# Optimization experiments

Measured on AMD Instinct MI355X. Metric: run time of the kernel, lower is better.

Reference implementation:

```python
import jax, jax.numpy as jnp
import numpy as np

EPS = 1e-5
STRIDE = 4
NSAMPLE = 8


def _fps(p, m):
    # furthest point sampling on one cloud p:[n,3] -> int32 indices [m]
    d0 = jnp.sum((p - p[0]) ** 2, axis=-1)
    def step(dist, _):
        nxt = jnp.argmax(dist).astype(jnp.int32)
        d = jnp.sum((p - p[nxt]) ** 2, axis=-1)
        return jnp.minimum(dist, d), nxt
    _, idxs = jax.lax.scan(step, d0, None, length=m - 1)
    return jnp.concatenate([jnp.zeros((1,), jnp.int32), idxs])


def _bn(x, gamma, beta):
    # inference-mode BatchNorm1d with running_mean=0, running_var=1
    return gamma * x / jnp.sqrt(1.0 + EPS) + beta


def _transition_down(p, x, W, gamma, beta):
    # p:[B,n,3], x:[B,n,C]  (stride>1 path of TransitionDown)
    B, n, _ = p.shape
    m = n // STRIDE
    pc = jax.lax.stop_gradient(p)
    idx = jax.vmap(_fps, in_axes=(0, None))(pc, m)              # [B,m]
    n_p = jnp.take_along_axis(p, idx[:, :, None], axis=1)       # [B,m,3]
    npc = jax.lax.stop_gradient(n_p)
    # squared distances sampled->all points, [B,m,n] (no [B,m,n,3] temp)
    d2 = (jnp.sum(npc ** 2, -1)[:, :, None]
          + jnp.sum(pc ** 2, -1)[:, None, :]
          - 2.0 * jnp.einsum('bmd,bnd->bmn', npc, pc))
    _, knn = jax.lax.top_k(-d2, NSAMPLE)                        # [B,m,k]
    gp = jax.vmap(lambda pb, kb: pb[kb])(p, knn)                # [B,m,k,3]
    gx = jax.vmap(lambda xb, kb: xb[kb])(x, knn)                # [B,m,k,C]
    rel = gp - n_p[:, :, None, :]                               # use_xyz=True
    feat = jnp.concatenate([rel, gx], axis=-1)                  # [B,m,k,3+C]
    y = jax.nn.relu(_bn(feat @ W, gamma, beta))
    return n_p, jnp.max(y, axis=2)                              # MaxPool1d(k)


def setup_inputs():
    key = jax.random.key(0)
    ks = jax.random.split(key, 16)
    B, n = 8, 8192
    N = B * n
    inp = {
        'p0': jax.random.normal(ks[0], (N, 3), jnp.float32),
        'x0': jax.random.normal(ks[1], (N, 3), jnp.float32),
        'o0': (jnp.arange(1, B + 1) * n).astype(jnp.int32),
    }
    dims_in = [6, 3 + 32, 3 + 64, 3 + 128, 3 + 256]
    dims_out = [32, 64, 128, 256, 512]
    for i in range(5):
        s = 1.0 / np.sqrt(dims_in[i])
        inp[f'W{i+1}'] = jax.random.uniform(ks[2 + i], (dims_in[i], dims_out[i]), jnp.float32, -s, s)
        inp[f'g{i+1}'] = jnp.ones((dims_out[i],), jnp.float32)
        inp[f'b{i+1}'] = jnp.zeros((dims_out[i],), jnp.float32)
    s1 = 1.0 / np.sqrt(512.0)
    inp['Wc1'] = jax.random.uniform(ks[8], (512, 256), jnp.float32, -s1, s1)
    inp['bc1'] = jax.random.uniform(ks[9], (256,), jnp.float32, -s1, s1)
    inp['gcls'] = jnp.ones((256,), jnp.float32)
    inp['bcls'] = jnp.zeros((256,), jnp.float32)
    s2 = 1.0 / np.sqrt(256.0)
    inp['Wc2'] = jax.random.uniform(ks[10], (256, 40), jnp.float32, -s2, s2)
    inp['bc2'] = jax.random.uniform(ks[11], (40,), jnp.float32, -s2, s2)
    return inp


def reference(p0, x0, o0, W1, g1, b1, W2, g2, b2, W3, g3, b3, W4, g4, b4,
              W5, g5, b5, Wc1, bc1, gcls, bcls, Wc2, bc2):
    B = o0.shape[0]
    n = p0.shape[0] // B  # equal-size segments
    p = p0.reshape(B, n, 3)
    x = jnp.concatenate([p0, x0], axis=1).reshape(B, n, 6)  # c=6: cat(xyz, feat)
    # enc1: stride 1 -> relu(bn(linear(x)))
    x = jax.nn.relu(_bn(x @ W1, g1, b1))
    # enc2..enc5: FPS + KNN group + linear/bn/relu + maxpool over neighbors
    p, x = _transition_down(p, x, W2, g2, b2)
    p, x = _transition_down(p, x, W3, g3, b3)
    p, x = _transition_down(p, x, W4, g4, b4)
    p, x = _transition_down(p, x, W5, g5, b5)
    # offset-based segment mean pooling (equal segments -> mean over axis 1)
    pooled = jnp.mean(x, axis=1)                               # [B,512]
    h = jax.nn.relu(_bn(pooled @ Wc1 + bc1, gcls, bcls))       # dropout eval=id
    return h @ Wc2 + bc2                                       # [B,40]
```

## Files before the change

### kernel.cpp

```cpp
#include <hip/hip_runtime.h>
#include <float.h>

#define BNI 0.9999950000374997f

__device__ __forceinline__ float sq3(float x, float y, float z) {
  return __fadd_rn(__fadd_rn(__fmul_rn(x, x), __fmul_rn(y, y)), __fmul_rn(z, z));
}

__device__ __forceinline__ int key_idx(double k) {
  return ~__double2loint(k);
}

template <int CTRL>
__device__ __forceinline__ double dpp_max(double k) {
  union { double d; int i[2]; } u, r;
  u.d = k;
  r.i[0] = __builtin_amdgcn_mov_dpp(u.i[0], CTRL, 0xF, 0xF, true);
  r.i[1] = __builtin_amdgcn_mov_dpp(u.i[1], CTRL, 0xF, 0xF, true);
  return fmax(k, r.d);
}
__device__ __forceinline__ double swz16_max(double k) {
  union { double d; int i[2]; } u, r;
  u.d = k;
  r.i[0] = __builtin_amdgcn_ds_swizzle(u.i[0], 0x401F);
  r.i[1] = __builtin_amdgcn_ds_swizzle(u.i[1], 0x401F);
  return fmax(k, r.d);
}
__device__ __forceinline__ double bperm32_max(double k, int lane) {
  union { double d; int i[2]; } u, r;
  u.d = k;
  int addr = ((lane ^ 32) << 2);
  r.i[0] = __builtin_amdgcn_ds_bpermute(addr, u.i[0]);
  r.i[1] = __builtin_amdgcn_ds_bpermute(addr, u.i[1]);
  return fmax(k, r.d);
}
__device__ __forceinline__ double wave_max_key(double k, int lane) {
  k = dpp_max<0xB1>(k);
  k = dpp_max<0x4E>(k);
  k = dpp_max<0x141>(k);
  k = dpp_max<0x140>(k);
  k = swz16_max(k);
  k = bperm32_max(k, lane);
  return k;
}

__global__ void k_prep(const float* __restrict__ p, float4* __restrict__ P4, int N) {
  int i = blockIdx.x * blockDim.x + threadIdx.x;
  if (i < N) {
    float x = p[3 * i], y = p[3 * i + 1], z = p[3 * i + 2];
    P4[i] = make_float4(x, y, z, sq3(x, y, z));
  }
}

__global__ __launch_bounds__(256) void k_enc1(
    const float* __restrict__ p0, const float* __restrict__ x0,
    const float* __restrict__ W, const float* __restrict__ g, const float* __restrict__ bt,
    float* __restrict__ X, int N) {
  int t = blockIdx.x * 256 + threadIdx.x;
  int pt = t >> 5, c = t & 31;
  if (pt >= N) return;
  float i0 = p0[pt * 3], i1 = p0[pt * 3 + 1], i2 = p0[pt * 3 + 2];
  float i3 = x0[pt * 3], i4 = x0[pt * 3 + 1], i5 = x0[pt * 3 + 2];
  float a = i0 * W[c] + i1 * W[32 + c] + i2 * W[64 + c] +
            i3 * W[96 + c] + i4 * W[128 + c] + i5 * W[160 + c];
  a = a * (g[c] * BNI) + bt[c];
  X[(size_t)pt * 32 + c] = fmaxf(a, 0.f);
}

__device__ __forceinline__ unsigned mpart3(unsigned x) {
  return (x & 1u) | ((x & 2u) << 2) | ((x & 4u) << 4);
}
__device__ __forceinline__ int cell_id(float4 v, const float* __restrict__ bb) {
  int cx = min(max((int)((v.x - bb[0]) * bb[3]), 0), 7);
  int cy = min(max((int)((v.y - bb[1]) * bb[4]), 0), 7);
  int cz = min(max((int)((v.z - bb[2]) * bb[5]), 0), 7);
  return (int)((mpart3(cx) << 2) | (mpart3(cy) << 1) | mpart3(cz));
}

__global__ __launch_bounds__(256) void k_bbox(const float4* __restrict__ P, int n,
                                              float* __restrict__ bb) {
  __shared__ float sm[6][4];
  int b = blockIdx.x, tid = threadIdx.x, lane = tid & 63, wid = tid >> 6;
  const float4* Pb = P + (size_t)b * n;
  float lx = FLT_MAX, hx = -FLT_MAX, ly = FLT_MAX, hy = -FLT_MAX, lz = FLT_MAX, hz = -FLT_MAX;
  for (int i = tid; i < n; i += 256) {
    float4 v = Pb[i];
    lx = fminf(lx, v.x); hx = fmaxf(hx, v.x);
    ly = fminf(ly, v.y); hy = fmaxf(hy, v.y);
    lz = fminf(lz, v.z); hz = fmaxf(hz, v.z);
  }
#pragma unroll
  for (int off = 1; off < 64; off <<= 1) {
    lx = fminf(lx, __shfl_xor(lx, off)); hx = fmaxf(hx, __shfl_xor(hx, off));
    ly = fminf(ly, __shfl_xor(ly, off)); hy = fmaxf(hy, __shfl_xor(hy, off));
    lz = fminf(lz, __shfl_xor(lz, off)); hz = fmaxf(hz, __shfl_xor(hz, off));
  }
  if (lane == 0) {
    sm[0][wid] = lx; sm[1][wid] = hx; sm[2][wid] = ly;
    sm[3][wid] = hy; sm[4][wid] = lz; sm[5][wid] = hz;
  }
  __syncthreads();
  if (tid == 0) {
    float LX = fminf(fminf(sm[0][0], sm[0][1]), fminf(sm[0][2], sm[0][3]));
    float HX = fmaxf(fmaxf(sm[1][0], sm[1][1]), fmaxf(sm[1][2], sm[1][3]));
    float LY = fminf(fminf(sm[2][0], sm[2][1]), fminf(sm[2][2], sm[2][3]));
    float HY = fmaxf(fmaxf(sm[3][0], sm[3][1]), fmaxf(sm[3][2], sm[3][3]));
    float LZ = fminf(fminf(sm[4][0], sm[4][1]), fminf(sm[4][2], sm[4][3]));
    float HZ = fmaxf(fmaxf(sm[5][0], sm[5][1]), fmaxf(sm[5][2], sm[5][3]));
    float ex = HX - LX, ey = HY - LY, ez = HZ - LZ;
    float* o = bb + b * 8;
    o[0] = LX; o[1] = LY; o[2] = LZ;
    o[3] = ex > 0.f ? 8.f / ex : 0.f;
    o[4] = ey > 0.f ? 8.f / ey : 0.f;
    o[5] = ez > 0.f ? 8.f / ez : 0.f;
  }
}

__global__ void k_hist(const float4* __restrict__ P, const float* __restrict__ bb,
                       int* __restrict__ hist, int n, int total) {
  int i = blockIdx.x * blockDim.x + threadIdx.x;
  if (i >= total) return;
  int b = i / n;
  int cid = cell_id(P[i], bb + b * 8);
  atomicAdd(&hist[b * 512 + cid], 1);
}

__global__ __launch_bounds__(512) void k_scan(const int* __restrict__ hist,
                                              int* __restrict__ cursor) {
  __shared__ int s[512];
  int b = blockIdx.x, t = threadIdx.x;
  int h = hist[b * 512 + t];
  s[t] = h;
  __syncthreads();
  for (int d = 1; d < 512; d <<= 1) {
    int v = (t >= d) ? s[t - d] : 0;
    __syncthreads();
    s[t] += v;
    __syncthreads();
  }
  cursor[b * 512 + t] = s[t] - h;
}

__global__ void k_scatter(const float4* __restrict__ P, const float* __restrict__ bb,
                          int* __restrict__ cursor, float4* __restrict__ Psort,
                          int n, int total) {
  int i = blockIdx.x * blockDim.x + threadIdx.x;
  if (i >= total) return;
  int b = i / n, il = i - b * n;
  float4 v = P[i];
  int cid = cell_id(v, bb + b * 8);
  int pos = atomicAdd(&cursor[b * 512 + cid], 1);
  Psort[(size_t)b * n + pos] = make_float4(v.x, v.y, v.z, __int_as_float(il));
}

template <int PT, int NW>
__global__ __launch_bounds__(64 * NW) void k_fps(
    const float4* __restrict__ Psort, const float4* __restrict__ Porig,
    int n, int m, int* __restrict__ out_idx) {
  __shared__ double keys[2][NW];
  const int b = blockIdx.x;
  const int tid = threadIdx.x;
  const int lane = tid & 63, wid = tid >> 6;
  const float4* PS = Psort + (size_t)b * n;
  const float4* PO = Porig + (size_t)b * n;

  float px[PT], py[PT], pz[PT], dist[PT];
  int ni[PT];
  const int base = wid * (64 * PT);
#pragma unroll
  for (int k = 0; k < PT; ++k) {
    float4 v = PS[base + k * 64 + lane];
    px[k] = v.x; py[k] = v.y; pz[k] = v.z;
    ni[k] = ~__float_as_int(v.w);
  }
  float lx = px[0], hx = px[0], ly = py[0], hy = py[0], lz = pz[0], hz = pz[0];
#pragma unroll
  for (int k = 1; k < PT; ++k) {
    lx = fminf(lx, px[k]); hx = fmaxf(hx, px[k]);
    ly = fminf(ly, py[k]); hy = fmaxf(hy, py[k]);
    lz = fminf(lz, pz[k]); hz = fmaxf(hz, pz[k]);
  }
#pragma unroll
  for (int off = 1; off < 64; off <<= 1) {
    lx = fminf(lx, __shfl_xor(lx, off)); hx = fmaxf(hx, __shfl_xor(hx, off));
    ly = fminf(ly, __shfl_xor(ly, off)); hy = fmaxf(hy, __shfl_xor(hy, off));
    lz = fminf(lz, __shfl_xor(lz, off)); hz = fmaxf(hz, __shfl_xor(hz, off));
  }
  if (tid == 0) out_idx[(size_t)b * m] = 0;

  float4 q = PO[0];
  double lk = -1.0;
#pragma unroll
  for (int k = 0; k < PT; ++k) {
    float dx = __fsub_rn(px[k], q.x), dy = __fsub_rn(py[k], q.y), dz = __fsub_rn(pz[k], q.z);
    float d = sq3(dx, dy, dz);
    dist[k] = d;
    lk = fmax(lk, __hiloint2double(__float_as_int(d), ni[k]));
  }
  double wkey = wave_max_key(lk, lane);

  for (int t = 1; t < m; ++t) {
    int buf = t & 1;
    if (lane == 0) keys[buf][wid] = wkey;
    __syncthreads();
    double kb = keys[buf][lane & (NW - 1)];
    if (NW >= 2)  kb = dpp_max<0xB1>(kb);
    if (NW >= 4)  kb = dpp_max<0x4E>(kb);
    if (NW >= 8)  kb = dpp_max<0x141>(kb);
    if (NW >= 16) kb = dpp_max<0x140>(kb);
    int wi = key_idx(kb);
    if (tid == 0) out_idx[(size_t)b * m + t] = wi;
    if (t + 1 >= m) break;
    float4 qq = PO[wi];
    float tx = fmaxf(fmaxf(__fsub_rn(lx, qq.x), __fsub_rn(qq.x, hx)), 0.f);
    float ty = fmaxf(fmaxf(__fsub_rn(ly, qq.y), __fsub_rn(qq.y, hy)), 0.f);
    float tz = fmaxf(fmaxf(__fsub_rn(lz, qq.z), __fsub_rn(qq.z, hz)), 0.f);
    float lb = sq3(tx, ty, tz);
    float wv = __uint_as_float((unsigned)__double2hiint(wkey));
    if (lb < wv) {
      double lk2 = -1.0;
#pragma unroll
      for (int k = 0; k < PT; ++k) {
        float dx = __fsub_rn(px[k], qq.x), dy = __fsub_rn(py[k], qq.y), dz = __fsub_rn(pz[k], qq.z);
        float d = sq3(dx, dy, dz);
        float nd = fminf(dist[k], d);
        dist[k] = nd;
        lk2 = fmax(lk2, __hiloint2double(__float_as_int(nd), ni[k]));
      }
      wkey = wave_max_key(lk2, lane);
    }
  }
}

__global__ void k_gather(const float4* __restrict__ Pin, const int* __restrict__ idx,
                         float4* __restrict__ Pout, int n, int m, int total) {
  int t = blockIdx.x * blockDim.x + threadIdx.x;
  if (t >= total) return;
  int b = t / m;
  Pout[t] = Pin[(size_t)b * n + idx[t]];
}

__global__ __launch_bounds__(256) void k_knn(
    const float4* __restrict__ Pq, const float4* __restrict__ Pc,
    int n, int m, int* __restrict__ knn) {
  int gw = (blockIdx.x * 256 + threadIdx.x) >> 6;
  int lane = threadIdx.x & 63;
  int b = gw / m;
  float4 q = Pq[gw];
  const float4* C = Pc + (size_t)b * n;
  float ad[8];
  int ai[8];
#pragma unroll
  for (int s = 0; s < 8; ++s) { ad[s] = FLT_MAX; ai[s] = 0x7fffffff; }
  for (int j = lane; j < n; j += 64) {
    float4 c = C[j];
    float dot = __fadd_rn(__fadd_rn(__fmul_rn(q.x, c.x), __fmul_rn(q.y, c.y)), __fmul_rn(q.z, c.z));
    float d2 = __fsub_rn(__fadd_rn(q.w, c.w), __fmul_rn(2.f, dot));
    if (d2 < ad[7] || (d2 == ad[7] && j < ai[7])) {
      float cd = d2; int ci = j;
#pragma unroll
      for (int s = 0; s < 8; ++s) {
        bool sw = (cd < ad[s]) || (cd == ad[s] && ci < ai[s]);
        float td = ad[s]; int ti = ai[s];
        ad[s] = sw ? cd : td; ai[s] = sw ? ci : ti;
        cd = sw ? td : cd;  ci = sw ? ti : ci;
      }
    }
  }
  int pos = 0;
  int* kout = knn + (size_t)gw * 8;
#pragma unroll
  for (int r = 0; r < 8; ++r) {
    float hv = FLT_MAX; int hi = 0x7fffffff;
#pragma unroll
    for (int s = 7; s >= 0; --s)
      if (pos == s) { hv = ad[s]; hi = ai[s]; }
    float v = hv; int ix = hi;
#pragma unroll
    for (int off = 1; off < 64; off <<= 1) {
      float ov = __shfl_xor(v, off);
      int oi = __shfl_xor(ix, off);
      if (ov < v || (ov == v && oi < ix)) { v = ov; ix = oi; }
    }
    if (hv == v && hi == ix) pos++;
    if (lane == 0) kout[r] = ix;
  }
}

template <int CINF, int COUT>
__global__ __launch_bounds__(COUT) void k_feat(
    const float4* __restrict__ Pq, const float4* __restrict__ Pc,
    const float* __restrict__ Xin, const int* __restrict__ knn,
    const float* __restrict__ W, const float* __restrict__ g, const float* __restrict__ bt,
    float* __restrict__ Xout, int n, int m) {
  constexpr int F = 3 + CINF;
  __shared__ float sf[8][F];
  int bi = blockIdx.x;
  int b = bi / m;
  int tid = threadIdx.x;
  float4 q = Pq[bi];
  const int* kn = knn + (size_t)bi * 8;
  if (tid < 8) {
    int nb = kn[tid];
    float4 c = Pc[(size_t)b * n + nb];
    sf[tid][0] = c.x - q.x;
    sf[tid][1] = c.y - q.y;
    sf[tid][2] = c.z - q.z;
  }
  for (int e = tid; e < 8 * CINF; e += COUT) {
    int k = e / CINF, j = e - k * CINF;
    int nb = kn[k];
    sf[k][3 + j] = Xin[((size_t)b * n + nb) * CINF + j];
  }
  __syncthreads();
  int c = tid;
  float acc[8] = {0.f, 0.f, 0.f, 0.f, 0.f, 0.f, 0.f, 0.f};
  for (int j = 0; j < F; ++j) {
    float w = W[(size_t)j * COUT + c];
#pragma unroll
    for (int k = 0; k < 8; ++k) acc[k] = fmaf(sf[k][j], w, acc[k]);
  }
  float sc = g[c] * BNI, bb = bt[c];
  float mx = 0.f;
#pragma unroll
  for (int k = 0; k < 8; ++k) mx = fmaxf(mx, fmaf(acc[k], sc, bb));
  Xout[(size_t)bi * COUT + c] = mx;
}

__global__ __launch_bounds__(512) void k_head(
    const float* __restrict__ X5, const float* __restrict__ Wc1, const float* __restrict__ bc1,
    const float* __restrict__ gc, const float* __restrict__ bcl,
    const float* __restrict__ Wc2, const float* __restrict__ bc2,
    float* __restrict__ out, int m5) {
  __shared__ float sp[512];
  __shared__ float sh[256];
  int b = blockIdx.x, tid = threadIdx.x;
  float s = 0.f;
  for (int i = 0; i < m5; ++i) s += X5[((size_t)b * m5 + i) * 512 + tid];
  sp[tid] = s * (1.0f / m5);
  __syncthreads();
  if (tid < 256) {
    float a = bc1[tid];
    for (int j = 0; j < 512; ++j) a = fmaf(sp[j], Wc1[j * 256 + tid], a);
    a = a * (gc[tid] * BNI) + bcl[tid];
    sh[tid] = fmaxf(a, 0.f);
  }
  __syncthreads();
  if (tid < 40) {
    float a = bc2[tid];
    for (int j = 0; j < 256; ++j) a = fmaf(sh[j], Wc2[j * 40 + tid], a);
    out[b * 40 + tid] = a;
  }
}

extern "C" void kernel_launch(void* const* d_in, const int* in_sizes, int n_in,
                              void* d_out, int out_size, void* d_ws, size_t ws_size,
                              hipStream_t stream) {
  const float* p0 = (const float*)d_in[0];
  const float* x0 = (const float*)d_in[1];
  const int B = in_sizes[2];
  const int N = in_sizes[0] / 3;
  const int n = N / B;
  const float* W1 = (const float*)d_in[3];
  const float* g1 = (const float*)d_in[4];
  const float* b1 = (const float*)d_in[5];
  const float* W2 = (const float*)d_in[6];
  const float* g2 = (const float*)d_in[7];
  const float* b2 = (const float*)d_in[8];
  const float* W3 = (const float*)d_in[9];
  const float* g3 = (const float*)d_in[10];
  const float* b3 = (const float*)d_in[11];
  const float* W4 = (const float*)d_in[12];
  const float* g4 = (const float*)d_in[13];
  const float* b4 = (const float*)d_in[14];
  const float* W5 = (const float*)d_in[15];
  const float* g5 = (const float*)d_in[16];
  const float* b5 = (const float*)d_in[17];
  const float* Wc1 = (const float*)d_in[18];
  const float* bc1 = (const float*)d_in[19];
  const float* gcls = (const float*)d_in[20];
  const float* bcls = (const float*)d_in[21];
  const float* Wc2 = (const float*)d_in[22];
  const float* bc2 = (const float*)d_in[23];
  float* out = (float*)d_out;

  const int m2 = n / 4, m3 = m2 / 4, m4 = m3 / 4, m5 = m4 / 4;

  char* ws = (char*)d_ws;
  size_t off = 0;
  auto alloc = [&](size_t bytes) -> void* {
    void* p = ws + off;
    off += (bytes + 255) & ~(size_t)255;
    return p;
  };
  float4* P2 = (float4*)alloc((size_t)N * 16);
  float* X1 = (float*)alloc((size_t)N * 32 * 4);
  float4* P3 = (float4*)alloc((size_t)B * m2 * 16);
  float4* P4s = (float4*)alloc((size_t)B * m3 * 16);
  float4* P5 = (float4*)alloc((size_t)B * m4 * 16);
  float4* P6 = (float4*)alloc((size_t)B * m5 * 16);
  int* fpsI = (int*)alloc((size_t)B * m2 * 4);
  int* knnI = (int*)alloc((size_t)B * m2 * 8 * 4);
  float* X2 = (float*)alloc((size_t)B * m2 * 64 * 4);
  float* X3 = (float*)alloc((size_t)B * m3 * 128 * 4);
  float* X4 = (float*)alloc((size_t)B * m4 * 256 * 4);
  float* X5 = (float*)alloc((size_t)B * m5 * 512 * 4);
  float4* Psort = (float4*)alloc((size_t)N * 16);
  float* bbox = (float*)alloc((size_t)B * 8 * 4);
  int* hist = (int*)alloc((size_t)B * 512 * 4);
  int* cursor = (int*)alloc((size_t)B * 512 * 4);

  auto sort_stage = [&](const float4* P, int ns) {
    int total = B * ns;
    hipMemsetAsync(hist, 0, (size_t)B * 512 * 4, stream);
    k_bbox<<<B, 256, 0, stream>>>(P, ns, bbox);
    k_hist<<<(total + 255) / 256, 256, 0, stream>>>(P, bbox, hist, ns, total);
    k_scan<<<B, 512, 0, stream>>>(hist, cursor);
    k_scatter<<<(total + 255) / 256, 256, 0, stream>>>(P, bbox, cursor, Psort, ns, total);
  };

  k_prep<<<(N + 255) / 256, 256, 0, stream>>>(p0, P2, N);
  k_enc1<<<(N * 32 + 255) / 256, 256, 0, stream>>>(p0, x0, W1, g1, b1, X1, N);

  sort_stage(P2, n);
  k_fps<8, 16><<<B, 1024, 0, stream>>>(Psort, P2, n, m2, fpsI);
  k_gather<<<(B * m2 + 255) / 256, 256, 0, stream>>>(P2, fpsI, P3, n, m2, B * m2);
  k_knn<<<(B * m2) / 4, 256, 0, stream>>>(P3, P2, n, m2, knnI);
  k_feat<32, 64><<<B * m2, 64, 0, stream>>>(P3, P2, X1, knnI, W2, g2, b2, X2, n, m2);

  sort_stage(P3, m2);
  k_fps<4, 8><<<B, 512, 0, stream>>>(Psort, P3, m2, m3, fpsI);
  k_gather<<<(B * m3 + 255) / 256, 256, 0, stream>>>(P3, fpsI, P4s, m2, m3, B * m3);
  k_knn<<<(B * m3) / 4, 256, 0, stream>>>(P4s, P3, m2, m3, knnI);
  k_feat<64, 128><<<B * m3, 128, 0, stream>>>(P4s, P3, X2, knnI, W3, g3, b3, X3, m2, m3);

  sort_stage(P4s, m3);
  k_fps<2, 4><<<B, 256, 0, stream>>>(Psort, P4s, m3, m4, fpsI);
  k_gather<<<(B * m4 + 255) / 256, 256, 0, stream>>>(P4s, fpsI, P5, m3, m4, B * m4);
  k_knn<<<(B * m4) / 4, 256, 0, stream>>>(P5, P4s, m3, m4, knnI);
  k_feat<128, 256><<<B * m4, 256, 0, stream>>>(P5, P4s, X3, knnI, W4, g4, b4, X4, m3, m4);

  sort_stage(P5, m4);
  k_fps<1, 2><<<B, 128, 0, stream>>>(Psort, P5, m4, m5, fpsI);
  k_gather<<<(B * m5 + 255) / 256, 256, 0, stream>>>(P5, fpsI, P6, m4, m5, B * m5);
  k_knn<<<(B * m5) / 4, 256, 0, stream>>>(P6, P5, m4, m5, knnI);
  k_feat<256, 512><<<B * m5, 512, 0, stream>>>(P6, P5, X4, knnI, W5, g5, b5, X5, m4, m5);

  k_head<<<B, 512, 0, stream>>>(X5, Wc1, bc1, gcls, bcls, Wc2, bc2, out, m5);
}
```

Baseline: 2.621 ms.

## Carry winner coordinates through LDS in FPS and use permlane swaps

The FPS loop now tracks each lane's argmax coordinates and broadcasts the wave winner's xyz into shared memory with its key. This removes the dependent global load of the selected point (PO[wi]) from the serial critical path of every iteration. The cross-row wave reduction uses permlane16/32 swap instructions in place of ds_swizzle and ds_bpermute, and the selected indices are buffered in LDS and written out once at the end. The cost is extra registers and selects in the inner loop, plus a fixed 2048-entry sidx array, which assumes m <= 2048.

```diff
diff --git a/kernel.cpp b/kernel.cpp
--- a/kernel.cpp
+++ b/kernel.cpp
@@ -3,13 +3,12 @@
 
 #define BNI 0.9999950000374997f
 
+typedef unsigned int v2u __attribute__((ext_vector_type(2)));
+
 __device__ __forceinline__ float sq3(float x, float y, float z) {
   return __fadd_rn(__fadd_rn(__fmul_rn(x, x), __fmul_rn(y, y)), __fmul_rn(z, z));
 }
 
-__device__ __forceinline__ int key_idx(double k) {
-  return ~__double2loint(k);
-}
 
 template <int CTRL>
 __device__ __forceinline__ double dpp_max(double k) {
@@ -19,28 +18,29 @@
   r.i[1] = __builtin_amdgcn_mov_dpp(u.i[1], CTRL, 0xF, 0xF, true);
   return fmax(k, r.d);
 }
-__device__ __forceinline__ double swz16_max(double k) {
-  union { double d; int i[2]; } u, r;
-  u.d = k;
-  r.i[0] = __builtin_amdgcn_ds_swizzle(u.i[0], 0x401F);
-  r.i[1] = __builtin_amdgcn_ds_swizzle(u.i[1], 0x401F);
-  return fmax(k, r.d);
-}
-__device__ __forceinline__ double bperm32_max(double k, int lane) {
-  union { double d; int i[2]; } u, r;
-  u.d = k;
-  int addr = ((lane ^ 32) << 2);
-  r.i[0] = __builtin_amdgcn_ds_bpermute(addr, u.i[0]);
-  r.i[1] = __builtin_amdgcn_ds_bpermute(addr, u.i[1]);
-  return fmax(k, r.d);
-}
-__device__ __forceinline__ double wave_max_key(double k, int lane) {
+__device__ __forceinline__ double pl16_kmax(double k) {
+  union { double d; unsigned i[2]; } u; u.d = k;
+  v2u a0 = __builtin_amdgcn_permlane16_swap(u.i[0], u.i[0], false, false);
+  v2u a1 = __builtin_amdgcn_permlane16_swap(u.i[1], u.i[1], false, false);
+  k = fmax(k, __hiloint2double((int)a1[0], (int)a0[0]));
+  k = fmax(k, __hiloint2double((int)a1[1], (int)a0[1]));
+  return k;
+}
+__device__ __forceinline__ double pl32_kmax(double k) {
+  union { double d; unsigned i[2]; } u; u.d = k;
+  v2u a0 = __builtin_amdgcn_permlane32_swap(u.i[0], u.i[0], false, false);
+  v2u a1 = __builtin_amdgcn_permlane32_swap(u.i[1], u.i[1], false, false);
+  k = fmax(k, __hiloint2double((int)a1[0], (int)a0[0]));
+  k = fmax(k, __hiloint2double((int)a1[1], (int)a0[1]));
+  return k;
+}
+__device__ __forceinline__ double wave_kmax(double k) {
   k = dpp_max<0xB1>(k);
   k = dpp_max<0x4E>(k);
   k = dpp_max<0x141>(k);
   k = dpp_max<0x140>(k);
-  k = swz16_max(k);
-  k = bperm32_max(k, lane);
+  k = pl16_kmax(k);
+  k = pl32_kmax(k);
   return k;
 }
 
@@ -157,7 +157,9 @@
 __global__ __launch_bounds__(64 * NW) void k_fps(
     const float4* __restrict__ Psort, const float4* __restrict__ Porig,
     int n, int m, int* __restrict__ out_idx) {
-  __shared__ double keys[2][NW];
+  __shared__ double skey[2][NW];
+  __shared__ float4 scrd[2][NW];
+  __shared__ int sidx[2048];
   const int b = blockIdx.x;
   const int tid = threadIdx.x;
   const int lane = tid & 63, wid = tid >> 6;
@@ -186,50 +188,80 @@
     ly = fminf(ly, __shfl_xor(ly, off)); hy = fmaxf(hy, __shfl_xor(hy, off));
     lz = fminf(lz, __shfl_xor(lz, off)); hz = fmaxf(hz, __shfl_xor(hz, off));
   }
-  if (tid == 0) out_idx[(size_t)b * m] = 0;
-
-  float4 q = PO[0];
+  if (tid == 0) sidx[0] = 0;
+
+  float4 q0 = PO[0];
   double lk = -1.0;
+  float cbx = 0.f, cby = 0.f, cbz = 0.f;
 #pragma unroll
   for (int k = 0; k < PT; ++k) {
-    float dx = __fsub_rn(px[k], q.x), dy = __fsub_rn(py[k], q.y), dz = __fsub_rn(pz[k], q.z);
+    float dx = __fsub_rn(px[k], q0.x), dy = __fsub_rn(py[k], q0.y), dz = __fsub_rn(pz[k], q0.z);
     float d = sq3(dx, dy, dz);
     dist[k] = d;
-    lk = fmax(lk, __hiloint2double(__float_as_int(d), ni[k]));
-  }
-  double wkey = wave_max_key(lk, lane);
+    double cand = __hiloint2double(__float_as_int(d), ni[k]);
+    if (cand > lk) { lk = cand; cbx = px[k]; cby = py[k]; cbz = pz[k]; }
+  }
+  double wk = wave_kmax(lk);
+  {
+    unsigned long long mkm = __ballot(__double_as_longlong(lk) == __double_as_longlong(wk));
+    int wl = (int)__ffsll((long long)mkm) - 1;
+    cbx = __int_as_float(__builtin_amdgcn_readlane(__float_as_int(cbx), wl));
+    cby = __int_as_float(__builtin_amdgcn_readlane(__float_as_int(cby), wl));
+    cbz = __int_as_float(__builtin_amdgcn_readlane(__float_as_int(cbz), wl));
+  }
+  if (lane == 0) {
+    skey[1][wid] = wk;
+    scrd[1][wid] = make_float4(cbx, cby, cbz, 0.f);
+  }
 
   for (int t = 1; t < m; ++t) {
     int buf = t & 1;
-    if (lane == 0) keys[buf][wid] = wkey;
     __syncthreads();
-    double kb = keys[buf][lane & (NW - 1)];
-    if (NW >= 2)  kb = dpp_max<0xB1>(kb);
-    if (NW >= 4)  kb = dpp_max<0x4E>(kb);
-    if (NW >= 8)  kb = dpp_max<0x141>(kb);
-    if (NW >= 16) kb = dpp_max<0x140>(kb);
-    int wi = key_idx(kb);
-    if (tid == 0) out_idx[(size_t)b * m + t] = wi;
+    int rs = lane & (NW - 1);
+    double mine = skey[buf][rs];
+    double ck = mine;
+    if (NW >= 2)  ck = dpp_max<0xB1>(ck);
+    if (NW >= 4)  ck = dpp_max<0x4E>(ck);
+    if (NW >= 8)  ck = dpp_max<0x141>(ck);
+    if (NW >= 16) ck = dpp_max<0x140>(ck);
+    if (tid == 0) sidx[t] = ~__double2loint(ck);
     if (t + 1 >= m) break;
-    float4 qq = PO[wi];
-    float tx = fmaxf(fmaxf(__fsub_rn(lx, qq.x), __fsub_rn(qq.x, hx)), 0.f);
-    float ty = fmaxf(fmaxf(__fsub_rn(ly, qq.y), __fsub_rn(qq.y, hy)), 0.f);
-    float tz = fmaxf(fmaxf(__fsub_rn(lz, qq.z), __fsub_rn(qq.z, hz)), 0.f);
+    unsigned long long wm = __ballot(__double_as_longlong(mine) == __double_as_longlong(ck));
+    int w = (int)__ffsll((long long)wm) - 1;
+    float4 qc = scrd[buf][w];
+    float tx = fmaxf(fmaxf(__fsub_rn(lx, qc.x), __fsub_rn(qc.x, hx)), 0.f);
+    float ty = fmaxf(fmaxf(__fsub_rn(ly, qc.y), __fsub_rn(qc.y, hy)), 0.f);
+    float tz = fmaxf(fmaxf(__fsub_rn(lz, qc.z), __fsub_rn(qc.z, hz)), 0.f);
     float lb = sq3(tx, ty, tz);
-    float wv = __uint_as_float((unsigned)__double2hiint(wkey));
+    float wv = __uint_as_float((unsigned)__double2hiint(wk));
     if (lb < wv) {
       double lk2 = -1.0;
+      float nbx = 0.f, nby = 0.f, nbz = 0.f;
 #pragma unroll
       for (int k = 0; k < PT; ++k) {
-        float dx = __fsub_rn(px[k], qq.x), dy = __fsub_rn(py[k], qq.y), dz = __fsub_rn(pz[k], qq.z);
+        float dx = __fsub_rn(px[k], qc.x), dy = __fsub_rn(py[k], qc.y), dz = __fsub_rn(pz[k], qc.z);
         float d = sq3(dx, dy, dz);
         float nd = fminf(dist[k], d);
         dist[k] = nd;
-        lk2 = fmax(lk2, __hiloint2double(__float_as_int(nd), ni[k]));
+        double cand = __hiloint2double(__float_as_int(nd), ni[k]);
+        if (cand > lk2) { lk2 = cand; nbx = px[k]; nby = py[k]; nbz = pz[k]; }
       }
-      wkey = wave_max_key(lk2, lane);
+      wk = wave_kmax(lk2);
+      unsigned long long mkm = __ballot(__double_as_longlong(lk2) == __double_as_longlong(wk));
+      int wl = (int)__ffsll((long long)mkm) - 1;
+      cbx = __int_as_float(__builtin_amdgcn_readlane(__float_as_int(nbx), wl));
+      cby = __int_as_float(__builtin_amdgcn_readlane(__float_as_int(nby), wl));
+      cbz = __int_as_float(__builtin_amdgcn_readlane(__float_as_int(nbz), wl));
     }
-  }
+    int nbuf = buf ^ 1;
+    if (lane == 0) {
+      skey[nbuf][wid] = wk;
+      scrd[nbuf][wid] = make_float4(cbx, cby, cbz, 0.f);
+    }
+  }
+  __syncthreads();
+  for (int i = tid; i < m; i += 64 * NW)
+    out_idx[(size_t)b * m + i] = sidx[i];
 }
 
 __global__ void k_gather(const float4* __restrict__ Pin, const int* __restrict__ idx,
```

New measurement: 3.016 ms. 1.15x slower.

## Co-schedule FPS with independent KNN/feature work in fused combo kernels

Applied to the files above, without the earlier changes.

Each stage's FPS kernel uses only B blocks and is serial, so the device sits mostly idle while it runs. Independent work (enc1, previous stage's KNN and feature MLP) is folded into the same launch as extra blocks so it runs concurrently with FPS. Feature kernels now also handle multiple queries per block to raise block size. The cost is extra shared memory and register pressure in the fused kernels, which could lower FPS occupancy or let the other blocks compete with FPS for the device.

```diff
diff --git a/kernel.cpp b/kernel.cpp
--- a/kernel.cpp
+++ b/kernel.cpp
@@ -7,9 +7,7 @@
   return __fadd_rn(__fadd_rn(__fmul_rn(x, x), __fmul_rn(y, y)), __fmul_rn(z, z));
 }
 
-__device__ __forceinline__ int key_idx(double k) {
-  return ~__double2loint(k);
-}
+__device__ __forceinline__ int key_idx(double k) { return ~__double2loint(k); }
 
 template <int CTRL>
 __device__ __forceinline__ double dpp_max(double k) {
@@ -50,21 +48,6 @@
     float x = p[3 * i], y = p[3 * i + 1], z = p[3 * i + 2];
     P4[i] = make_float4(x, y, z, sq3(x, y, z));
   }
-}
-
-__global__ __launch_bounds__(256) void k_enc1(
-    const float* __restrict__ p0, const float* __restrict__ x0,
-    const float* __restrict__ W, const float* __restrict__ g, const float* __restrict__ bt,
-    float* __restrict__ X, int N) {
-  int t = blockIdx.x * 256 + threadIdx.x;
-  int pt = t >> 5, c = t & 31;
-  if (pt >= N) return;
-  float i0 = p0[pt * 3], i1 = p0[pt * 3 + 1], i2 = p0[pt * 3 + 2];
-  float i3 = x0[pt * 3], i4 = x0[pt * 3 + 1], i5 = x0[pt * 3 + 2];
-  float a = i0 * W[c] + i1 * W[32 + c] + i2 * W[64 + c] +
-            i3 * W[96 + c] + i4 * W[128 + c] + i5 * W[160 + c];
-  a = a * (g[c] * BNI) + bt[c];
-  X[(size_t)pt * 32 + c] = fmaxf(a, 0.f);
 }
 
 __device__ __forceinline__ unsigned mpart3(unsigned x) {
@@ -154,11 +137,9 @@
 }
 
 template <int PT, int NW>
-__global__ __launch_bounds__(64 * NW) void k_fps(
+__device__ __forceinline__ void fps_body(
     const float4* __restrict__ Psort, const float4* __restrict__ Porig,
-    int n, int m, int* __restrict__ out_idx) {
-  __shared__ double keys[2][NW];
-  const int b = blockIdx.x;
+    int n, int m, int* __restrict__ out_idx, int b, double* keys ) {
   const int tid = threadIdx.x;
   const int lane = tid & 63, wid = tid >> 6;
   const float4* PS = Psort + (size_t)b * n;
@@ -188,11 +169,11 @@
   }
   if (tid == 0) out_idx[(size_t)b * m] = 0;
 
-  float4 q = PO[0];
+  float4 q0 = PO[0];
   double lk = -1.0;
 #pragma unroll
   for (int k = 0; k < PT; ++k) {
-    float dx = __fsub_rn(px[k], q.x), dy = __fsub_rn(py[k], q.y), dz = __fsub_rn(pz[k], q.z);
+    float dx = __fsub_rn(px[k], q0.x), dy = __fsub_rn(py[k], q0.y), dz = __fsub_rn(pz[k], q0.z);
     float d = sq3(dx, dy, dz);
     dist[k] = d;
     lk = fmax(lk, __hiloint2double(__float_as_int(d), ni[k]));
@@ -201,9 +182,9 @@
 
   for (int t = 1; t < m; ++t) {
     int buf = t & 1;
-    if (lane == 0) keys[buf][wid] = wkey;
+    if (lane == 0) keys[buf * 16 + wid] = wkey;
     __syncthreads();
-    double kb = keys[buf][lane & (NW - 1)];
+    double kb = keys[buf * 16 + (lane & (NW - 1))];
     if (NW >= 2)  kb = dpp_max<0xB1>(kb);
     if (NW >= 4)  kb = dpp_max<0x4E>(kb);
     if (NW >= 8)  kb = dpp_max<0x141>(kb);
@@ -232,18 +213,22 @@
   }
 }
 
-__global__ void k_gather(const float4* __restrict__ Pin, const int* __restrict__ idx,
-                         float4* __restrict__ Pout, int n, int m, int total) {
-  int t = blockIdx.x * blockDim.x + threadIdx.x;
-  if (t >= total) return;
-  int b = t / m;
-  Pout[t] = Pin[(size_t)b * n + idx[t]];
-}
-
-__global__ __launch_bounds__(256) void k_knn(
-    const float4* __restrict__ Pq, const float4* __restrict__ Pc,
-    int n, int m, int* __restrict__ knn) {
-  int gw = (blockIdx.x * 256 + threadIdx.x) >> 6;
+__device__ __forceinline__ void enc1_body(
+    const float* __restrict__ p0, const float* __restrict__ x0,
+    const float* __restrict__ W, const float* __restrict__ g,
+    const float* __restrict__ bt, float* __restrict__ X, int N, int t) {
+  int pt = t >> 5, c = t & 31;
+  if (pt >= N) return;
+  float i0 = p0[pt * 3], i1 = p0[pt * 3 + 1], i2 = p0[pt * 3 + 2];
+  float i3 = x0[pt * 3], i4 = x0[pt * 3 + 1], i5 = x0[pt * 3 + 2];
+  float a = i0 * W[c] + i1 * W[32 + c] + i2 * W[64 + c] +
+            i3 * W[96 + c] + i4 * W[128 + c] + i5 * W[160 + c];
+  a = a * (g[c] * BNI) + bt[c];
+  X[(size_t)pt * 32 + c] = fmaxf(a, 0.f);
+}
+
+__device__ void knn_body(const float4* __restrict__ Pq, const float4* __restrict__ Pc,
+                         int n, int m, int* __restrict__ knn, int gw) {
   int lane = threadIdx.x & 63;
   int b = gw / m;
   float4 q = Pq[gw];
@@ -287,44 +272,167 @@
   }
 }
 
-template <int CINF, int COUT>
-__global__ __launch_bounds__(COUT) void k_feat(
+template <int CINF, int COUT, int NT>
+__device__ __forceinline__ void feat_body(
     const float4* __restrict__ Pq, const float4* __restrict__ Pc,
     const float* __restrict__ Xin, const int* __restrict__ knn,
-    const float* __restrict__ W, const float* __restrict__ g, const float* __restrict__ bt,
-    float* __restrict__ Xout, int n, int m) {
+    const float* __restrict__ W, const float* __restrict__ g,
+    const float* __restrict__ bt, float* __restrict__ Xout,
+    int n, int m, int bi0, int total, char* smem) {
   constexpr int F = 3 + CINF;
-  __shared__ float sf[8][F];
-  int bi = blockIdx.x;
-  int b = bi / m;
+  constexpr int NQ = NT / COUT;
+  typedef float SF[8][F];
+  SF* sf = (SF*)smem;
   int tid = threadIdx.x;
-  float4 q = Pq[bi];
-  const int* kn = knn + (size_t)bi * 8;
-  if (tid < 8) {
-    int nb = kn[tid];
-    float4 c = Pc[(size_t)b * n + nb];
-    sf[tid][0] = c.x - q.x;
-    sf[tid][1] = c.y - q.y;
-    sf[tid][2] = c.z - q.z;
-  }
-  for (int e = tid; e < 8 * CINF; e += COUT) {
-    int k = e / CINF, j = e - k * CINF;
-    int nb = kn[k];
-    sf[k][3 + j] = Xin[((size_t)b * n + nb) * CINF + j];
+  if (tid < NQ * 8) {
+    int ql = tid >> 3, k = tid & 7;
+    int bi = bi0 + ql;
+    if (bi < total) {
+      float4 q = Pq[bi];
+      int b = bi / m;
+      int nb = knn[(size_t)bi * 8 + k];
+      float4 c = Pc[(size_t)b * n + nb];
+      sf[ql][k][0] = c.x - q.x;
+      sf[ql][k][1] = c.y - q.y;
+      sf[ql][k][2] = c.z - q.z;
+    }
+  }
+  for (int e = tid; e < NQ * 8 * CINF; e += NT) {
+    int ql = e / (8 * CINF);
+    int r = e - ql * (8 * CINF);
+    int k = r / CINF, j = r - k * CINF;
+    int bi = bi0 + ql;
+    if (bi < total) {
+      int b = bi / m;
+      int nb = knn[(size_t)bi * 8 + k];
+      sf[ql][k][3 + j] = Xin[((size_t)b * n + nb) * CINF + j];
+    }
   }
   __syncthreads();
-  int c = tid;
+  int ql = tid / COUT, c = tid - ql * COUT;
+  int bi = bi0 + ql;
+  if (bi >= total) return;
   float acc[8] = {0.f, 0.f, 0.f, 0.f, 0.f, 0.f, 0.f, 0.f};
   for (int j = 0; j < F; ++j) {
     float w = W[(size_t)j * COUT + c];
 #pragma unroll
-    for (int k = 0; k < 8; ++k) acc[k] = fmaf(sf[k][j], w, acc[k]);
+    for (int k = 0; k < 8; ++k) acc[k] = fmaf(sf[ql][k][j], w, acc[k]);
   }
   float sc = g[c] * BNI, bb = bt[c];
   float mx = 0.f;
 #pragma unroll
   for (int k = 0; k < 8; ++k) mx = fmaxf(mx, fmaf(acc[k], sc, bb));
   Xout[(size_t)bi * COUT + c] = mx;
+}
+
+__global__ __launch_bounds__(1024) void k_combo0(
+    const float4* __restrict__ Psort, const float4* __restrict__ P2,
+    int n, int m2, int* __restrict__ fpsI,
+    const float* __restrict__ p0, const float* __restrict__ x0,
+    const float* __restrict__ W1, const float* __restrict__ g1,
+    const float* __restrict__ b1, float* __restrict__ X1, int N, int B) {
+  __shared__ double skeys[32];
+  int bid = blockIdx.x;
+  if (bid < B) { fps_body<8, 16>(Psort, P2, n, m2, fpsI, bid, skeys); return; }
+  enc1_body(p0, x0, W1, g1, b1, X1, N, (bid - B) * 1024 + threadIdx.x);
+}
+
+__global__ __launch_bounds__(512) void k_combo1(
+    const float4* __restrict__ Psort, const float4* __restrict__ P3,
+    int m2, int m3, int* __restrict__ fpsI,
+    const float4* __restrict__ P2, int n, int* __restrict__ knnA,
+    int B, int totq) {
+  __shared__ double skeys[32];
+  int bid = blockIdx.x;
+  if (bid < B) { fps_body<4, 8>(Psort, P3, m2, m3, fpsI, bid, skeys); return; }
+  int gw = (bid - B) * 8 + (threadIdx.x >> 6);
+  if (gw < totq) knn_body(P3, P2, n, m2, knnA, gw);
+}
+
+__global__ __launch_bounds__(256) void k_combo2(
+    const float4* __restrict__ Psort, const float4* __restrict__ P4s,
+    int m3, int m4, int* __restrict__ fpsI,
+    const float4* __restrict__ P3, int m2, int* __restrict__ knnB,
+    const float4* __restrict__ P2, const float* __restrict__ X1,
+    const int* __restrict__ knnA,
+    const float* __restrict__ W2, const float* __restrict__ g2,
+    const float* __restrict__ b2, float* __restrict__ X2,
+    int n, int B, int nkb, int totq3, int totq2) {
+  __shared__ double skeys[32];
+  __shared__ __align__(16) char sfm[4480];
+  int bid = blockIdx.x;
+  if (bid < B) { fps_body<2, 4>(Psort, P4s, m3, m4, fpsI, bid, skeys); return; }
+  bid -= B;
+  if (bid < nkb) {
+    int gw = bid * 4 + (threadIdx.x >> 6);
+    if (gw < totq3) knn_body(P4s, P3, m2, m3, knnB, gw);
+    return;
+  }
+  bid -= nkb;
+  feat_body<32, 64, 256>(P3, P2, X1, knnA, W2, g2, b2, X2, n, m2,
+                         bid * 4, totq2, sfm);
+}
+
+__global__ __launch_bounds__(128) void k_combo3(
+    const float4* __restrict__ Psort, const float4* __restrict__ P5,
+    int m4, int m5, int* __restrict__ fpsI,
+    const float4* __restrict__ P4s, int m3, int* __restrict__ knnA,
+    const float4* __restrict__ P3, const float* __restrict__ X2,
+    const int* __restrict__ knnB,
+    const float* __restrict__ W3, const float* __restrict__ g3,
+    const float* __restrict__ b3, float* __restrict__ X3,
+    int m2, int B, int nkb, int totq4, int totq3) {
+  __shared__ double skeys[32];
+  __shared__ __align__(16) char sfm[2144];
+  int bid = blockIdx.x;
+  if (bid < B) { fps_body<1, 2>(Psort, P5, m4, m5, fpsI, bid, skeys); return; }
+  bid -= B;
+  if (bid < nkb) {
+    int gw = bid * 2 + (threadIdx.x >> 6);
+    if (gw < totq4) knn_body(P5, P4s, m3, m4, knnA, gw);
+    return;
+  }
+  bid -= nkb;
+  feat_body<64, 128, 128>(P4s, P3, X2, knnB, W3, g3, b3, X3, m2, m3,
+                          bid, totq3, sfm);
+}
+
+__global__ __launch_bounds__(512) void k_combo4(
+    const float4* __restrict__ P6, const float4* __restrict__ P5,
+    int m4, int m5, int* __restrict__ knnB,
+    const float4* __restrict__ P4s, const float* __restrict__ X3,
+    const int* __restrict__ knnA,
+    const float* __restrict__ W4, const float* __restrict__ g4,
+    const float* __restrict__ b4, float* __restrict__ X4,
+    int m3, int nkb, int totq5, int totq4) {
+  __shared__ __align__(16) char sfm[8384];
+  int bid = blockIdx.x;
+  if (bid < nkb) {
+    int gw = bid * 8 + (threadIdx.x >> 6);
+    if (gw < totq5) knn_body(P6, P5, m4, m5, knnB, gw);
+    return;
+  }
+  bid -= nkb;
+  feat_body<128, 256, 512>(P5, P4s, X3, knnA, W4, g4, b4, X4, m3, m4,
+                           bid * 2, totq4, sfm);
+}
+
+__global__ void k_gather(const float4* __restrict__ Pin, const int* __restrict__ idx,
+                         float4* __restrict__ Pout, int n, int m, int total) {
+  int t = blockIdx.x * blockDim.x + threadIdx.x;
+  if (t >= total) return;
+  int b = t / m;
+  Pout[t] = Pin[(size_t)b * n + idx[t]];
+}
+
+__global__ __launch_bounds__(512) void k_feat5(
+    const float4* __restrict__ Pq, const float4* __restrict__ Pc,
+    const float* __restrict__ Xin, const int* __restrict__ knn,
+    const float* __restrict__ W, const float* __restrict__ g,
+    const float* __restrict__ bt, float* __restrict__ Xout, int n, int m) {
+  __shared__ __align__(16) char sfm[8 * 259 * 4];
+  feat_body<256, 512, 512>(Pq, Pc, Xin, knn, W, g, bt, Xout, n, m,
+                           blockIdx.x, gridDim.x, sfm);
 }
 
 __global__ __launch_bounds__(512) void k_head(
@@ -400,7 +508,8 @@
   float4* P5 = (float4*)alloc((size_t)B * m4 * 16);
   float4* P6 = (float4*)alloc((size_t)B * m5 * 16);
   int* fpsI = (int*)alloc((size_t)B * m2 * 4);
-  int* knnI = (int*)alloc((size_t)B * m2 * 8 * 4);
+  int* knnA = (int*)alloc((size_t)B * m2 * 8 * 4);
+  int* knnB = (int*)alloc((size_t)B * m3 * 8 * 4);
   float* X2 = (float*)alloc((size_t)B * m2 * 64 * 4);
   float* X3 = (float*)alloc((size_t)B * m3 * 128 * 4);
   float* X4 = (float*)alloc((size_t)B * m4 * 256 * 4);
@@ -420,31 +529,51 @@
   };
 
   k_prep<<<(N + 255) / 256, 256, 0, stream>>>(p0, P2, N);
-  k_enc1<<<(N * 32 + 255) / 256, 256, 0, stream>>>(p0, x0, W1, g1, b1, X1, N);
 
   sort_stage(P2, n);
-  k_fps<8, 16><<<B, 1024, 0, stream>>>(Psort, P2, n, m2, fpsI);
+  {
+    int eb = (N * 32 + 1023) / 1024;
+    k_combo0<<<B + eb, 1024, 0, stream>>>(Psort, P2, n, m2, fpsI,
+                                          p0, x0, W1, g1, b1, X1, N, B);
+  }
   k_gather<<<(B * m2 + 255) / 256, 256, 0, stream>>>(P2, fpsI, P3, n, m2, B * m2);
-  k_knn<<<(B * m2) / 4, 256, 0, stream>>>(P3, P2, n, m2, knnI);
-  k_feat<32, 64><<<B * m2, 64, 0, stream>>>(P3, P2, X1, knnI, W2, g2, b2, X2, n, m2);
 
   sort_stage(P3, m2);
-  k_fps<4, 8><<<B, 512, 0, stream>>>(Psort, P3, m2, m3, fpsI);
+  {
+    int kb = (B * m2 + 7) / 8;
+    k_combo1<<<B + kb, 512, 0, stream>>>(Psort, P3, m2, m3, fpsI,
+                                         P2, n, knnA, B, B * m2);
+  }
   k_gather<<<(B * m3 + 255) / 256, 256, 0, stream>>>(P3, fpsI, P4s, m2, m3, B * m3);
-  k_knn<<<(B * m3) / 4, 256, 0, stream>>>(P4s, P3, m2, m3, knnI);
-  k_feat<64, 128><<<B * m3, 128, 0, stream>>>(P4s, P3, X2, knnI, W3, g3, b3, X3, m2, m3);
 
   sort_stage(P4s, m3);
-  k_fps<2, 4><<<B, 256, 0, stream>>>(Psort, P4s, m3, m4, fpsI);
+  {
+    int nkb = (B * m3 + 3) / 4;
+    int fb = (B * m2 + 3) / 4;
+    k_combo2<<<B + nkb + fb, 256, 0, stream>>>(
+        Psort, P4s, m3, m4, fpsI, P3, m2, knnB, P2, X1, knnA,
+        W2, g2, b2, X2, n, B, nkb, B * m3, B * m2);
+  }
   k_gather<<<(B * m4 + 255) / 256, 256, 0, stream>>>(P4s, fpsI, P5, m3, m4, B * m4);
-  k_knn<<<(B * m4) / 4, 256, 0, stream>>>(P5, P4s, m3, m4, knnI);
-  k_feat<128, 256><<<B * m4, 256, 0, stream>>>(P5, P4s, X3, knnI, W4, g4, b4, X4, m3, m4);
 
   sort_stage(P5, m4);
-  k_fps<1, 2><<<B, 128, 0, stream>>>(Psort, P5, m4, m5, fpsI);
+  {
+    int nkb = (B * m4 + 1) / 2;
+    int fb = B * m3;
+    k_combo3<<<B + nkb + fb, 128, 0, stream>>>(
+        Psort, P5, m4, m5, fpsI, P4s, m3, knnA, P3, X2, knnB,
+        W3, g3, b3, X3, m2, B, nkb, B * m4, B * m3);
+  }
   k_gather<<<(B * m5 + 255) / 256, 256, 0, stream>>>(P5, fpsI, P6, m4, m5, B * m5);
-  k_knn<<<(B * m5) / 4, 256, 0, stream>>>(P6, P5, m4, m5, knnI);
-  k_feat<256, 512><<<B * m5, 512, 0, stream>>>(P6, P5, X4, knnI, W5, g5, b5, X5, m4, m5);
-
+
+  {
+    int nkb = (B * m5 + 7) / 8;
+    int fb = (B * m4 + 1) / 2;
+    k_combo4<<<nkb + fb, 512, 0, stream>>>(
+        P6, P5, m4, m5, knnB, P4s, X3, knnA,
+        W4, g4, b4, X4, m3, nkb, B * m5, B * m4);
+  }
+
+  k_feat5<<<B * m5, 512, 0, stream>>>(P6, P5, X4, knnB, W5, g5, b5, X5, m4, m5);
   k_head<<<B, 512, 0, stream>>>(X5, Wc1, bc1, gcls, bcls, Wc2, bc2, out, m5);
 }
```

After: 2.259 ms. 13.8% less time.
